# Performance work log

Hardware: AMD Instinct MI355X
Metric: run time of the kernel (lower is better)

The kernel has to match this reference:

```python
import jax, jax.numpy as jnp
import numpy as np

B, T, D, C = 8, 4096, 768, 2048

def setup_inputs() -> dict:
    key = jax.random.key(0)
    k1, k2 = jax.random.split(key)
    embed = jax.random.normal(k1, (B, T, D), dtype=jnp.float32)
    cluster_centers = jax.random.normal(k2, (C, D), dtype=jnp.float32)
    return {"embed": embed, "cluster_centers": cluster_centers}

def reference(embed, cluster_centers):
    x_sq = jnp.sum(embed * embed, axis=-1, keepdims=True)          # (b, t, 1)
    c_sq = jnp.sum(cluster_centers * cluster_centers, axis=-1)     # (c,)
    cross = jnp.einsum('btd,cd->btc', embed, cluster_centers)      # (b, t, c)
    sq_dists = x_sq + c_sq[None, None, :] - 2.0 * cross
    dists = jnp.sqrt(jnp.maximum(sq_dists, 0.0))
    # dists argmax of -cdist == argmin of cdist
    clusters = jnp.argmin(dists, axis=-1)                          # (b, t) int
    return clusters
```

## Files before the change

### kernel.cpp

```cpp
#include <hip/hip_runtime.h>

typedef __fp16 f16x2 __attribute__((ext_vector_type(2)));
typedef __fp16 f16x8 __attribute__((ext_vector_type(8)));
typedef float f32x4 __attribute__((ext_vector_type(4)));

constexpr int MM = 32768;
constexpr int NN = 2048;
constexpr int KK = 768;
constexpr int NKT = KK / 32;
constexpr int NA_UNITS = (MM / 16) * NKT;
constexpr int NB_UNITS = (NN / 16) * NKT;

constexpr size_t WS_APACK = 0;
constexpr size_t WS_BPACK = WS_APACK + (size_t)MM * KK * 4;
constexpr size_t WS_CSQ   = WS_BPACK + (size_t)NN * KK * 4;
constexpr size_t WS_SLOT  = WS_CSQ + (size_t)NN * 4;
constexpr size_t WS_NEED  = WS_SLOT + (size_t)MM * 16 * 8;

__device__ __forceinline__ unsigned bc(f16x2 h) {
    return __builtin_bit_cast(unsigned, h);
}


__global__ __launch_bounds__(256)
void fragpack_kernel(const float* __restrict__ A, const float* __restrict__ Bc,
                     uint4* __restrict__ Ap, uint4* __restrict__ Bp,
                     float* __restrict__ csq) {
    const int task = blockIdx.x * 4 + (threadIdx.x >> 6);
    const int lane = threadIdx.x & 63;

    if (task >= NA_UNITS + NB_UNITS) {
        const int cl = task - (NA_UNITS + NB_UNITS);
        const float4* row = reinterpret_cast<const float4*>(Bc + (size_t)cl * KK);
        float s = 0.f;
#pragma unroll
        for (int w = 0; w < KK / (4 * 64); ++w) {
            float4 v = row[w * 64 + lane];
            s = fmaf(v.x, v.x, s); s = fmaf(v.y, v.y, s);
            s = fmaf(v.z, v.z, s); s = fmaf(v.w, v.w, s);
        }
#pragma unroll
        for (int off = 32; off > 0; off >>= 1) s += __shfl_xor(s, off, 64);
        if (lane == 0) csq[cl] = s;
        return;
    }

    const int ln15 = lane & 15;
    const int quad = lane >> 4;

    const bool isB = task >= NA_UNITS;
    const int t = isB ? task - NA_UNITS : task;
    const int tile = t / NKT, kt = t % NKT;
    const float* src = (isB ? Bc : A) + (size_t)(tile * 16 + ln15) * KK + kt * 32 + quad * 8;
    uint4* dst = (isB ? Bp : Ap) + (size_t)t * 128 + lane;

    const float4 v0 = *(const float4*)(src);
    const float4 v1 = *(const float4*)(src + 4);
    f16x2 h0 = __builtin_amdgcn_cvt_pkrtz(v0.x, v0.y);
    f16x2 h1 = __builtin_amdgcn_cvt_pkrtz(v0.z, v0.w);
    f16x2 h2 = __builtin_amdgcn_cvt_pkrtz(v1.x, v1.y);
    f16x2 h3 = __builtin_amdgcn_cvt_pkrtz(v1.z, v1.w);
    f16x2 l0 = __builtin_amdgcn_cvt_pkrtz(v0.x-(float)h0[0], v0.y-(float)h0[1]);
    f16x2 l1 = __builtin_amdgcn_cvt_pkrtz(v0.z-(float)h1[0], v0.w-(float)h1[1]);
    f16x2 l2 = __builtin_amdgcn_cvt_pkrtz(v1.x-(float)h2[0], v1.y-(float)h2[1]);
    f16x2 l3 = __builtin_amdgcn_cvt_pkrtz(v1.z-(float)h3[0], v1.w-(float)h3[1]);
    uint4 hv = {bc(h0), bc(h1), bc(h2), bc(h3)};
    uint4 lv = {bc(l0), bc(l1), bc(l2), bc(l3)};
    dst[0]  = hv;
    dst[64] = lv;
}

__global__ __launch_bounds__(64)
void csq_kernel(const float* __restrict__ cc, float* __restrict__ csq) {
    const int cl = blockIdx.x;
    const int lane = threadIdx.x;
    const float4* row = reinterpret_cast<const float4*>(cc + (size_t)cl * KK);
    float s = 0.f;
#pragma unroll
    for (int w = 0; w < KK / (4 * 64); ++w) {
        float4 v = row[w * 64 + lane];
        s = fmaf(v.x, v.x, s); s = fmaf(v.y, v.y, s);
        s = fmaf(v.z, v.z, s); s = fmaf(v.w, v.w, s);
    }
#pragma unroll
    for (int off = 32; off > 0; off >>= 1) s += __shfl_xor(s, off, 64);
    if (lane == 0) csq[cl] = s;
}

#define MF2(a, b, c) __builtin_amdgcn_mfma_f32_16x16x32_f16(a, b, c, 0, 0, 0)
#define DSB() __builtin_amdgcn_sched_barrier(0)

__global__ __launch_bounds__(256, 2)
void gemm_pack_kernel(const uint4* __restrict__ Ap, const uint4* __restrict__ Bp,
                      const float* __restrict__ csq, uint2* __restrict__ slots) {
    __shared__ uint4 ldsq[4096];

    const int b   = blockIdx.x;
    const int xcd = b & 7;
    const int s   = b >> 3;
    const int gx  = s & 15;
    const int gy  = xcd + ((s >> 4) << 3);

    const int tid  = threadIdx.x;
    const int lane = tid & 63;
    const int ln15 = lane & 15;
    const int quad = lane >> 4;
    const int wave = tid >> 6;
    const int wm   = wave >> 1;
    const int wn   = wave & 1;
    const int tbase = gy * 128;
    const int cb    = gx * 128;

    const uint4* sp[8];
#pragma unroll
    for (int q = 0; q < 8; ++q) {
        const int u = wave * 8 + q;
        const bool isA = u < 16;
        const int v = isA ? u : u - 16;
        const int tile = (isA ? gy * 8 : gx * 8) + (v >> 1);
        const int part = v & 1;
        sp[q] = (isA ? Ap : Bp) + (size_t)tile * NKT * 128 + part * 64 + lane;
    }

#define STAGE_ALL(kt_, bufq_) { if ((kt_) < NKT) {                            \
    _Pragma("unroll")                                                         \
    for (int qq = 0; qq < 8; ++qq)                                            \
        __builtin_amdgcn_global_load_lds(                                     \
            (const __attribute__((address_space(1))) unsigned int*)(sp[qq] + (kt_) * 128), \
            (__attribute__((address_space(3))) unsigned int*)&ldsq[(bufq_) + (wave * 8 + qq) * 64], \
            16, 0, 0); } }

#define RD_SET(Ah_, Al_, Bh_, Bl_, bufq_) {                                   \
    _Pragma("unroll")                                                         \
    for (int j = 0; j < 4; ++j) {                                             \
        const int nu = 16 + (wn * 4 + j) * 2;                                 \
        Bh_[j] = *(const f16x8*)&ldsq[(bufq_) + nu * 64 + lane];              \
        Bl_[j] = *(const f16x8*)&ldsq[(bufq_) + (nu + 1) * 64 + lane];        \
    }                                                                         \
    _Pragma("unroll")                                                         \
    for (int i = 0; i < 4; ++i) {                                             \
        const int au = (wm * 4 + i) * 2;                                      \
        Ah_[i] = *(const f16x8*)&ldsq[(bufq_) + au * 64 + lane];              \
        Al_[i] = *(const f16x8*)&ldsq[(bufq_) + (au + 1) * 64 + lane];        \
    } }

#define MFMA_I2(Ah_, Al_, Bh_, Bl_, i_) {                                     \
    _Pragma("unroll")                                                         \
    for (int j = 0; j < 4; ++j) acc[i_][j] = MF2(Ah_[i_], Bh_[j], acc[i_][j]);\
    _Pragma("unroll")                                                         \
    for (int j = 0; j < 4; ++j) acc[i_][j] = MF2(Ah_[i_], Bl_[j], acc[i_][j]);\
    _Pragma("unroll")                                                         \
    for (int j = 0; j < 4; ++j) acc[i_][j] = MF2(Al_[i_], Bh_[j], acc[i_][j]);\
}

#define WAIT_VM0()   { asm volatile("s_waitcnt vmcnt(0)" ::: "memory"); DSB(); }
#define WAIT_LGKM0() { asm volatile("s_waitcnt lgkmcnt(0)" ::: "memory"); DSB(); }
#define BARRIER()    { DSB(); __builtin_amdgcn_s_barrier(); DSB(); }

    f32x4 acc[4][4];
#pragma unroll
    for (int i = 0; i < 4; ++i)
#pragma unroll
        for (int j = 0; j < 4; ++j) { f32x4 z = {0.f,0.f,0.f,0.f}; acc[i][j] = z; }

    f16x8 Ah0[4], Al0[4], Bh0[4], Bl0[4];
    f16x8 Ah1[4], Al1[4], Bh1[4], Bl1[4];

    STAGE_ALL(0, 0)
    WAIT_VM0(); BARRIER();
    RD_SET(Ah0, Al0, Bh0, Bl0, 0)
    STAGE_ALL(1, 2048)
    WAIT_LGKM0();

#pragma unroll 1
    for (int kt = 0; kt < NKT; kt += 2) {
        MFMA_I2(Ah0, Al0, Bh0, Bl0, 0)
        MFMA_I2(Ah0, Al0, Bh0, Bl0, 1)
        DSB();
        WAIT_VM0(); BARRIER();
        RD_SET(Ah1, Al1, Bh1, Bl1, 2048)
        STAGE_ALL(kt + 2, 0)
        DSB();
        MFMA_I2(Ah0, Al0, Bh0, Bl0, 2)
        MFMA_I2(Ah0, Al0, Bh0, Bl0, 3)
        DSB();
        WAIT_LGKM0();

        MFMA_I2(Ah1, Al1, Bh1, Bl1, 0)
        MFMA_I2(Ah1, Al1, Bh1, Bl1, 1)
        DSB();
        WAIT_VM0(); BARRIER();
        if (kt + 2 < NKT) { RD_SET(Ah0, Al0, Bh0, Bl0, 0) }
        STAGE_ALL(kt + 3, 2048)
        DSB();
        MFMA_I2(Ah1, Al1, Bh1, Bl1, 2)
        MFMA_I2(Ah1, Al1, Bh1, Bl1, 3)
        DSB();
        WAIT_LGKM0();
    }

    float csq4[4];
#pragma unroll
    for (int j = 0; j < 4; ++j) csq4[j] = csq[cb + wn * 64 + j * 16 + ln15];

    float bval[16]; int bidx[16];
#pragma unroll
    for (int i = 0; i < 4; ++i)
#pragma unroll
        for (int r = 0; r < 4; ++r) {
            const int rid = i * 4 + r;
            float bv_ = csq4[0] - 2.0f * acc[i][0][r];
            int   bi_ = cb + wn * 64 + ln15;
#pragma unroll
            for (int j = 1; j < 4; ++j) {
                const float s2 = csq4[j] - 2.0f * acc[i][j][r];
                const int   c = cb + wn * 64 + j * 16 + ln15;
                if (s2 < bv_) { bv_ = s2; bi_ = c; }
            }
            bval[rid] = bv_; bidx[rid] = bi_;
        }
#pragma unroll
    for (int off = 1; off < 16; off <<= 1) {
#pragma unroll
        for (int rid = 0; rid < 16; ++rid) {
            const float ov = __shfl_xor(bval[rid], off, 64);
            const int   oi = __shfl_xor(bidx[rid], off, 64);
            if (ov < bval[rid] || (ov == bval[rid] && oi < bidx[rid])) {
                bval[rid] = ov; bidx[rid] = oi;
            }
        }
    }

    __syncthreads();
    float* vtab = (float*)&ldsq[0];
    int*   itab = (int*)&ldsq[64];
    if (ln15 == 0) {
#pragma unroll
        for (int i = 0; i < 4; ++i)
#pragma unroll
            for (int r = 0; r < 4; ++r) {
                const int row = wm * 64 + i * 16 + quad * 4 + r;
                vtab[row * 2 + wn] = bval[i * 4 + r];
                itab[row * 2 + wn] = bidx[i * 4 + r];
            }
    }
    __syncthreads();
    if (tid < 128) {
        float v0 = vtab[tid * 2]; int i0 = itab[tid * 2];
        const float v1 = vtab[tid * 2 + 1]; const int i1 = itab[tid * 2 + 1];
        if (v1 < v0 || (v1 == v0 && i1 < i0)) { v0 = v1; i0 = i1; }
        uint2 e; e.x = __float_as_uint(v0); e.y = (unsigned)i0;
        slots[(size_t)(tbase + tid) * 16 + gx] = e;
    }
}

__global__ __launch_bounds__(256)
void slot_reduce_kernel(const uint2* __restrict__ slots, int* __restrict__ out) {
    const int t = blockIdx.x * 256 + threadIdx.x;
    const uint2* s = slots + (size_t)t * 16;
    float bv = __uint_as_float(s[0].x); int bi = (int)s[0].y;
#pragma unroll
    for (int j = 1; j < 16; ++j) {
        const uint2 e = s[j];
        const float v = __uint_as_float(e.x);
        if (v < bv || (v == bv && (int)e.y < bi)) { bv = v; bi = (int)e.y; }
    }
    out[t] = bi;
}


__global__ __launch_bounds__(256)
void init_ws_kernel(unsigned long long* __restrict__ w) {
    w[blockIdx.x * 256 + threadIdx.x] = 0xFFFFFFFFFFFFFFFFull;
}

__global__ __launch_bounds__(256, 2)
void argmin_mfma_kernel(const float* __restrict__ A, const float* __restrict__ Bc,
                        const float* __restrict__ csq,
                        unsigned long long* __restrict__ ws64) {
    __shared__ unsigned lds[4 * 128 * 20];
    constexpr int AH = 0, AL = 2560, BH = 5120;

    const int tid  = threadIdx.x;
    const int lane = tid & 63;
    const int ln15 = lane & 15;
    const int quad = lane >> 4;
    const int wave = tid >> 6;
    const int wm = wave >> 1, wn = wave & 1;
    const int tbase = blockIdx.x * 128;
    const int cb    = blockIdx.y * 128;

    const int sr  = tid >> 1;
    const int skh = tid & 1;
    const float* gA = A  + (size_t)(tbase + sr) * KK + skh * 16;
    const float* gB = Bc + (size_t)(cb   + sr) * KK + skh * 16;
    const int wword = sr * 20 + skh * 8;

    f32x4 acc[4][4];
#pragma unroll
    for (int i = 0; i < 4; ++i)
#pragma unroll
        for (int j = 0; j < 4; ++j) { f32x4 z = {0.f,0.f,0.f,0.f}; acc[i][j] = z; }

    float4 av[4], bv[4];
#pragma unroll
    for (int p = 0; p < 4; ++p) {
        av[p] = *(const float4*)(gA + p * 4);
        bv[p] = *(const float4*)(gB + p * 4);
    }

    int aw[4], bw[4];
#pragma unroll
    for (int i = 0; i < 4; ++i) {
        aw[i] = AH + (wm * 64 + i * 16 + ln15) * 20 + quad * 4;
        bw[i] = BH + (wn * 64 + i * 16 + ln15) * 20 + quad * 4;
    }

    for (int k0 = 0; k0 < KK; k0 += 32) {
        __syncthreads();
#pragma unroll
        for (int h = 0; h < 2; ++h) {
            float4 v0 = av[2*h], v1 = av[2*h+1];
            f16x2 h00 = __builtin_amdgcn_cvt_pkrtz(v0.x, v0.y);
            f16x2 h01 = __builtin_amdgcn_cvt_pkrtz(v0.z, v0.w);
            f16x2 h10 = __builtin_amdgcn_cvt_pkrtz(v1.x, v1.y);
            f16x2 h11 = __builtin_amdgcn_cvt_pkrtz(v1.z, v1.w);
            f16x2 l00 = __builtin_amdgcn_cvt_pkrtz(v0.x-(float)h00[0], v0.y-(float)h00[1]);
            f16x2 l01 = __builtin_amdgcn_cvt_pkrtz(v0.z-(float)h01[0], v0.w-(float)h01[1]);
            f16x2 l10 = __builtin_amdgcn_cvt_pkrtz(v1.x-(float)h10[0], v1.y-(float)h10[1]);
            f16x2 l11 = __builtin_amdgcn_cvt_pkrtz(v1.z-(float)h11[0], v1.w-(float)h11[1]);
            uint4 hv = {bc(h00), bc(h01), bc(h10), bc(h11)};
            uint4 lv = {bc(l00), bc(l01), bc(l10), bc(l11)};
            *(uint4*)&lds[AH + wword + 4*h] = hv;
            *(uint4*)&lds[AL + wword + 4*h] = lv;

            float4 w0 = bv[2*h], w1 = bv[2*h+1];
            f16x2 g00 = __builtin_amdgcn_cvt_pkrtz(w0.x, w0.y);
            f16x2 g01 = __builtin_amdgcn_cvt_pkrtz(w0.z, w0.w);
            f16x2 g10 = __builtin_amdgcn_cvt_pkrtz(w1.x, w1.y);
            f16x2 g11 = __builtin_amdgcn_cvt_pkrtz(w1.z, w1.w);
            f16x2 m00 = __builtin_amdgcn_cvt_pkrtz(w0.x-(float)g00[0], w0.y-(float)g00[1]);
            f16x2 m01 = __builtin_amdgcn_cvt_pkrtz(w0.z-(float)g01[0], w0.w-(float)g01[1]);
            f16x2 m10 = __builtin_amdgcn_cvt_pkrtz(w1.x-(float)g10[0], w1.y-(float)g10[1]);
            f16x2 m11 = __builtin_amdgcn_cvt_pkrtz(w1.z-(float)g11[0], w1.w-(float)g11[1]);
            uint4 gv = {bc(g00), bc(g01), bc(g10), bc(g11)};
            uint4 mv = {bc(m00), bc(m01), bc(m10), bc(m11)};
            *(uint4*)&lds[BH + wword + 4*h]        = gv;
            *(uint4*)&lds[BH + 2560 + wword + 4*h] = mv;
        }
        __syncthreads();

        const int kn = k0 + 32;
        if (kn < KK) {
#pragma unroll
            for (int p = 0; p < 4; ++p) {
                av[p] = *(const float4*)(gA + kn + p * 4);
                bv[p] = *(const float4*)(gB + kn + p * 4);
            }
        }

        f16x8 a_h[4], a_l[4], b_h[4], b_l[4];
#pragma unroll
        for (int i = 0; i < 4; ++i) {
            a_h[i] = *(const f16x8*)&lds[aw[i]];
            a_l[i] = *(const f16x8*)&lds[aw[i] + 2560];
            b_h[i] = *(const f16x8*)&lds[bw[i]];
            b_l[i] = *(const f16x8*)&lds[bw[i] + 2560];
        }
#pragma unroll
        for (int i = 0; i < 4; ++i)
#pragma unroll
            for (int j = 0; j < 4; ++j) {
                acc[i][j] = __builtin_amdgcn_mfma_f32_16x16x32_f16(a_h[i], b_h[j], acc[i][j], 0, 0, 0);
                acc[i][j] = __builtin_amdgcn_mfma_f32_16x16x32_f16(a_h[i], b_l[j], acc[i][j], 0, 0, 0);
                acc[i][j] = __builtin_amdgcn_mfma_f32_16x16x32_f16(a_l[i], b_h[j], acc[i][j], 0, 0, 0);
            }
    }

    float csq4[4];
#pragma unroll
    for (int j = 0; j < 4; ++j) csq4[j] = csq[cb + wn * 64 + j * 16 + ln15];

    float bval[16]; int bidx[16];
#pragma unroll
    for (int i = 0; i < 4; ++i)
#pragma unroll
        for (int r = 0; r < 4; ++r) {
            const int rid = i * 4 + r;
            float bv_ = csq4[0] - 2.0f * acc[i][0][r];
            int   bi_ = cb + wn * 64 + ln15;
#pragma unroll
            for (int j = 1; j < 4; ++j) {
                const float s = csq4[j] - 2.0f * acc[i][j][r];
                const int   c = cb + wn * 64 + j * 16 + ln15;
                if (s < bv_) { bv_ = s; bi_ = c; }
            }
            bval[rid] = bv_; bidx[rid] = bi_;
        }
#pragma unroll
    for (int off = 1; off < 16; off <<= 1) {
#pragma unroll
        for (int rid = 0; rid < 16; ++rid) {
            const float ov = __shfl_xor(bval[rid], off, 64);
            const int   oi = __shfl_xor(bidx[rid], off, 64);
            if (ov < bval[rid] || (ov == bval[rid] && oi < bidx[rid])) {
                bval[rid] = ov; bidx[rid] = oi;
            }
        }
    }

    __syncthreads();
    float* vtab = (float*)&lds[0];
    int*   itab = (int*)&lds[256];
    if (ln15 == 0) {
#pragma unroll
        for (int i = 0; i < 4; ++i)
#pragma unroll
            for (int r = 0; r < 4; ++r) {
                const int row = wm * 64 + i * 16 + quad * 4 + r;
                vtab[row * 2 + wn] = bval[i * 4 + r];
                itab[row * 2 + wn] = bidx[i * 4 + r];
            }
    }
    __syncthreads();
    if (tid < 128) {
        float v0 = vtab[tid * 2]; int i0 = itab[tid * 2];
        const float v1 = vtab[tid * 2 + 1]; const int i1 = itab[tid * 2 + 1];
        if (v1 < v0 || (v1 == v0 && i1 < i0)) { v0 = v1; i0 = i1; }
        const unsigned b   = __float_as_uint(v0);
        const unsigned key = (b & 0x80000000u) ? ~b : (b | 0x80000000u);
        const unsigned long long pk =
            ((unsigned long long)key << 32) | (unsigned long long)(unsigned)i0;
        atomicMin(&ws64[tbase + tid], pk);
    }
}

__global__ __launch_bounds__(256)
void unpack_kernel(const unsigned long long* __restrict__ w, int* __restrict__ out) {
    const int i = blockIdx.x * 256 + threadIdx.x;
    out[i] = (int)(unsigned)(w[i] & 0xFFFFFFFFull);
}

extern "C" void kernel_launch(void* const* d_in, const int* in_sizes, int n_in,
                              void* d_out, int out_size, void* d_ws, size_t ws_size,
                              hipStream_t stream) {
    const float* embed   = (const float*)d_in[0];
    const float* centers = (const float*)d_in[1];
    int* out = (int*)d_out;

    if (ws_size >= WS_NEED) {
        uint4* Ap = (uint4*)((char*)d_ws + WS_APACK);
        uint4* Bp = (uint4*)((char*)d_ws + WS_BPACK);
        float* csq   = (float*)((char*)d_ws + WS_CSQ);
        uint2* slots = (uint2*)((char*)d_ws + WS_SLOT);
        fragpack_kernel<<<(NA_UNITS + NB_UNITS + NN) / 4, 256, 0, stream>>>(
            embed, centers, Ap, Bp, csq);
        gemm_pack_kernel<<<(MM / 128) * (NN / 128), 256, 0, stream>>>(
            Ap, Bp, csq, slots);
        slot_reduce_kernel<<<MM / 256, 256, 0, stream>>>(slots, out);
    } else {
        unsigned long long* ws64 = (unsigned long long*)d_ws;
        float* csq = (float*)((char*)d_ws + (size_t)MM * 8);
        init_ws_kernel<<<MM / 256, 256, 0, stream>>>(ws64);
        csq_kernel<<<NN, 64, 0, stream>>>(centers, csq);
        argmin_mfma_kernel<<<dim3(MM / 128, NN / 128), 256, 0, stream>>>(
            embed, centers, csq, ws64);
        unpack_kernel<<<MM / 256, 256, 0, stream>>>(ws64, out);
    }
}
```

Measured before the change: 456.1 us.

## Single-buffer LDS and register fragments to raise GEMM occupancy to three blocks

Halves the LDS staging buffer and drops the second set of register fragments, so the K loop becomes single-stage: read all fragments, run the first MFMA group, barrier, issue the next tile's global-to-LDS loads, finish the MFMAs, then wait and barrier. The launch bound goes from 2 to 3 blocks per CU. The aim is to hide latency with more resident waves instead of software double buffering, at the cost of an exposed global load wait and two barriers per K step.

```diff
diff --git a/kernel.cpp b/kernel.cpp
--- a/kernel.cpp
+++ b/kernel.cpp
@@ -90,10 +90,10 @@
 #define MF2(a, b, c) __builtin_amdgcn_mfma_f32_16x16x32_f16(a, b, c, 0, 0, 0)
 #define DSB() __builtin_amdgcn_sched_barrier(0)
 
-__global__ __launch_bounds__(256, 2)
+__global__ __launch_bounds__(256, 3)
 void gemm_pack_kernel(const uint4* __restrict__ Ap, const uint4* __restrict__ Bp,
                       const float* __restrict__ csq, uint2* __restrict__ slots) {
-    __shared__ uint4 ldsq[4096];
+    __shared__ uint4 ldsq[2048];
 
     const int b   = blockIdx.x;
     const int xcd = b & 7;
@@ -122,81 +122,65 @@
         sp[q] = (isA ? Ap : Bp) + (size_t)tile * NKT * 128 + part * 64 + lane;
     }
 
-#define STAGE_ALL(kt_, bufq_) { if ((kt_) < NKT) {                            \
+#define STAGE_ALL(kt_) { if ((kt_) < NKT) {                                   \
     _Pragma("unroll")                                                         \
     for (int qq = 0; qq < 8; ++qq)                                            \
         __builtin_amdgcn_global_load_lds(                                     \
             (const __attribute__((address_space(1))) unsigned int*)(sp[qq] + (kt_) * 128), \
-            (__attribute__((address_space(3))) unsigned int*)&ldsq[(bufq_) + (wave * 8 + qq) * 64], \
+            (__attribute__((address_space(3))) unsigned int*)&ldsq[(wave * 8 + qq) * 64], \
             16, 0, 0); } }
 
-#define RD_SET(Ah_, Al_, Bh_, Bl_, bufq_) {                                   \
+    f32x4 acc[4][4];
+#pragma unroll
+    for (int i = 0; i < 4; ++i)
+#pragma unroll
+        for (int j = 0; j < 4; ++j) { f32x4 z = {0.f,0.f,0.f,0.f}; acc[i][j] = z; }
+
+    f16x8 Bh[4], Bl[4], Ah[4], Al[4];
+
+#define RD_ALL() {                                                            \
     _Pragma("unroll")                                                         \
     for (int j = 0; j < 4; ++j) {                                             \
         const int nu = 16 + (wn * 4 + j) * 2;                                 \
-        Bh_[j] = *(const f16x8*)&ldsq[(bufq_) + nu * 64 + lane];              \
-        Bl_[j] = *(const f16x8*)&ldsq[(bufq_) + (nu + 1) * 64 + lane];        \
+        Bh[j] = *(const f16x8*)&ldsq[nu * 64 + lane];                         \
+        Bl[j] = *(const f16x8*)&ldsq[(nu + 1) * 64 + lane];                   \
     }                                                                         \
     _Pragma("unroll")                                                         \
     for (int i = 0; i < 4; ++i) {                                             \
         const int au = (wm * 4 + i) * 2;                                      \
-        Ah_[i] = *(const f16x8*)&ldsq[(bufq_) + au * 64 + lane];              \
-        Al_[i] = *(const f16x8*)&ldsq[(bufq_) + (au + 1) * 64 + lane];        \
+        Ah[i] = *(const f16x8*)&ldsq[au * 64 + lane];                         \
+        Al[i] = *(const f16x8*)&ldsq[(au + 1) * 64 + lane];                   \
     } }
 
-#define MFMA_I2(Ah_, Al_, Bh_, Bl_, i_) {                                     \
-    _Pragma("unroll")                                                         \
-    for (int j = 0; j < 4; ++j) acc[i_][j] = MF2(Ah_[i_], Bh_[j], acc[i_][j]);\
-    _Pragma("unroll")                                                         \
-    for (int j = 0; j < 4; ++j) acc[i_][j] = MF2(Ah_[i_], Bl_[j], acc[i_][j]);\
-    _Pragma("unroll")                                                         \
-    for (int j = 0; j < 4; ++j) acc[i_][j] = MF2(Al_[i_], Bh_[j], acc[i_][j]);\
+#define MFMA_I2(i_) {                                                         \
+    _Pragma("unroll")                                                         \
+    for (int j = 0; j < 4; ++j) acc[i_][j] = MF2(Ah[i_], Bh[j], acc[i_][j]);  \
+    _Pragma("unroll")                                                         \
+    for (int j = 0; j < 4; ++j) acc[i_][j] = MF2(Ah[i_], Bl[j], acc[i_][j]);  \
+    _Pragma("unroll")                                                         \
+    for (int j = 0; j < 4; ++j) acc[i_][j] = MF2(Al[i_], Bh[j], acc[i_][j]);  \
 }
 
 #define WAIT_VM0()   { asm volatile("s_waitcnt vmcnt(0)" ::: "memory"); DSB(); }
 #define WAIT_LGKM0() { asm volatile("s_waitcnt lgkmcnt(0)" ::: "memory"); DSB(); }
 #define BARRIER()    { DSB(); __builtin_amdgcn_s_barrier(); DSB(); }
 
-    f32x4 acc[4][4];
-#pragma unroll
-    for (int i = 0; i < 4; ++i)
-#pragma unroll
-        for (int j = 0; j < 4; ++j) { f32x4 z = {0.f,0.f,0.f,0.f}; acc[i][j] = z; }
-
-    f16x8 Ah0[4], Al0[4], Bh0[4], Bl0[4];
-    f16x8 Ah1[4], Al1[4], Bh1[4], Bl1[4];
-
-    STAGE_ALL(0, 0)
+    STAGE_ALL(0)
     WAIT_VM0(); BARRIER();
-    RD_SET(Ah0, Al0, Bh0, Bl0, 0)
-    STAGE_ALL(1, 2048)
-    WAIT_LGKM0();
 
 #pragma unroll 1
-    for (int kt = 0; kt < NKT; kt += 2) {
-        MFMA_I2(Ah0, Al0, Bh0, Bl0, 0)
-        MFMA_I2(Ah0, Al0, Bh0, Bl0, 1)
+    for (int kt = 0; kt < NKT; ++kt) {
+        RD_ALL()
+        MFMA_I2(0)
+        WAIT_LGKM0();
+        BARRIER();
+        STAGE_ALL(kt + 1)
         DSB();
-        WAIT_VM0(); BARRIER();
-        RD_SET(Ah1, Al1, Bh1, Bl1, 2048)
-        STAGE_ALL(kt + 2, 0)
-        DSB();
-        MFMA_I2(Ah0, Al0, Bh0, Bl0, 2)
-        MFMA_I2(Ah0, Al0, Bh0, Bl0, 3)
-        DSB();
-        WAIT_LGKM0();
-
-        MFMA_I2(Ah1, Al1, Bh1, Bl1, 0)
-        MFMA_I2(Ah1, Al1, Bh1, Bl1, 1)
-        DSB();
-        WAIT_VM0(); BARRIER();
-        if (kt + 2 < NKT) { RD_SET(Ah0, Al0, Bh0, Bl0, 0) }
-        STAGE_ALL(kt + 3, 2048)
-        DSB();
-        MFMA_I2(Ah1, Al1, Bh1, Bl1, 2)
-        MFMA_I2(Ah1, Al1, Bh1, Bl1, 3)
-        DSB();
-        WAIT_LGKM0();
+        MFMA_I2(1)
+        MFMA_I2(2)
+        MFMA_I2(3)
+        WAIT_VM0();
+        BARRIER();
     }
 
     float csq4[4];
```

After: 435.4 us. 4.6% less time.
